# Kernel tuning notes

Measured on AMD Instinct MI355X. Metric: run time of the kernel, lower is better.

## Reference

```python
import jax, jax.numpy as jnp
import numpy as np

B, T, D, R, V = 8, 512, 1024, 4, 2048


def setup_inputs() -> dict:
    key = jax.random.key(0)
    k1, k2, k3, k4, k5 = jax.random.split(key, 5)
    return {
        "input_embs": jax.random.normal(k1, (B, T, D), dtype=jnp.float32),
        "label_ids": jax.random.randint(k2, (B, T), 0, V),
        "w_alpha": jax.random.normal(k3, (D, R), dtype=jnp.float32),
        "w_beta": jax.random.normal(k4, (D, R), dtype=jnp.float32),
        "w_vocab": jax.random.normal(k5, (D, V * R * R), dtype=jnp.float32),
    }


def _normalize(m, axis):
    # torch normalize_matrix: abs then divide by sum over `dim` (rows of the matrix)
    m = jnp.abs(m)
    return m / m.sum(axis=axis, keepdims=True)


def reference(input_embs, label_ids, w_alpha, w_beta, w_vocab):
    x = input_embs
    Bq, Tq, Dq = x.shape
    xf = x.reshape(-1, Dq)                                   # [B*T, D]
    alpha = (xf @ w_alpha).reshape(Bq, Tq, R).mean(1)        # [B, R]
    beta = (xf @ w_beta).reshape(Bq, Tq, R).mean(1)          # [B, R]
    core = (xf @ w_vocab).reshape(Bq, Tq, R, V, R).mean(1)   # [B, R, V, R]

    # gather core slices core[b, :, y[b,k], :] -> [B, T, R, R]
    g = jnp.take_along_axis(core.transpose(0, 2, 1, 3),      # [B, V, R, R]
                            label_ids[:, :, None, None], axis=1)
    Mn = _normalize(g, axis=2)                               # normalize over matrix rows (dim=0)

    v = _normalize(alpha, axis=1)                            # [B, R] normalized column vector
    Ms = Mn.transpose(1, 0, 2, 3)                            # [T, B, R, R]

    def step(v, M):
        return jnp.einsum('bij,bj->bi', M, v), None

    v, _ = jax.lax.scan(step, v, Ms)                         # sequential TT chain over T
    nb = _normalize(beta, axis=1)                            # [B, R]
    probs = jnp.einsum('bi,bi->b', nb, v)                    # [B]
    loss = -jnp.log(probs)
    return loss.mean()
```

## Files before the change

### kernel.cpp

```cpp
#include <hip/hip_runtime.h>
#include <math.h>

#define Bq 8
#define T 512
#define D 1024
#define R 4
#define V 2048
#define NCOL (V * R * R)
#define DSPLIT 16
#define DCHUNK (D / DSPLIT)
#define CBLK 1024

__global__ void k_xbar(const float* __restrict__ x, float* __restrict__ xbar) {
    int b   = blockIdx.x;
    int tc  = blockIdx.y;
    int tid = threadIdx.x;
    const float4* xp = (const float4*)(x + ((size_t)b * T + (size_t)tc * 16) * D) + tid;
    float4 acc = make_float4(0.f, 0.f, 0.f, 0.f);
#pragma unroll
    for (int t = 0; t < 16; ++t) {
        float4 v = xp[t * (D / 4)];
        acc.x += v.x; acc.y += v.y; acc.z += v.z; acc.w += v.w;
    }
    float* dst = xbar + b * D + tid * 4;
    atomicAdd(dst + 0, acc.x);
    atomicAdd(dst + 1, acc.y);
    atomicAdd(dst + 2, acc.z);
    atomicAdd(dst + 3, acc.w);
}

__global__ void k_core(const float* __restrict__ wv, const float* __restrict__ xbar,
                       float* __restrict__ part) {
    __shared__ float xs[Bq * DCHUNK];
    int tid  = threadIdx.x;
    int colb = blockIdx.x;
    int ds   = blockIdx.y;
    int d0   = ds * DCHUNK;

    if (tid < (Bq * DCHUNK / 4)) {
        int l  = tid * 4;
        int b  = l / DCHUNK;
        int dd = l % DCHUNK;
        *(float4*)(xs + l) = *(const float4*)(xbar + b * D + d0 + dd);
    }
    __syncthreads();

    int col = colb * CBLK + tid * 4;
    const float4* wp = (const float4*)(wv + (size_t)d0 * NCOL + col);
    float4 acc[Bq];
#pragma unroll
    for (int b = 0; b < Bq; ++b) acc[b] = make_float4(0.f, 0.f, 0.f, 0.f);

#pragma unroll 8
    for (int d = 0; d < DCHUNK; ++d) {
        float4 w = wp[(size_t)d * (NCOL / 4)];
#pragma unroll
        for (int b = 0; b < Bq; ++b) {
            float xv = xs[b * DCHUNK + d];
            acc[b].x += w.x * xv;
            acc[b].y += w.y * xv;
            acc[b].z += w.z * xv;
            acc[b].w += w.w * xv;
        }
    }

#pragma unroll
    for (int b = 0; b < Bq; ++b)
        *(float4*)(part + ((size_t)ds * Bq + b) * NCOL + col) = acc[b];
}

__global__ void k_gather(const float* __restrict__ part, const int* __restrict__ labels,
                         float* __restrict__ Mn) {
    int b   = blockIdx.x;
    int tc  = blockIdx.y;
    int tid = threadIdx.x;
    int tl  = tid >> 2;
    int i   = tid & 3;
    int t   = tc * 64 + tl;
    int y   = labels[b * T + t];

    const float* pb = part + (size_t)b * NCOL + (size_t)i * (V * R) + (size_t)y * R;
    float4 g = make_float4(0.f, 0.f, 0.f, 0.f);
#pragma unroll
    for (int ds = 0; ds < DSPLIT; ++ds) {
        float4 v = *(const float4*)(pb + (size_t)ds * (Bq * NCOL));
        g.x += v.x; g.y += v.y; g.z += v.z; g.w += v.w;
    }
    g.x = fabsf(g.x); g.y = fabsf(g.y); g.z = fabsf(g.z); g.w = fabsf(g.w);

    float sx = g.x, sy = g.y, sz = g.z, sw = g.w;
    sx += __shfl_xor(sx, 1); sy += __shfl_xor(sy, 1);
    sz += __shfl_xor(sz, 1); sw += __shfl_xor(sw, 1);
    sx += __shfl_xor(sx, 2); sy += __shfl_xor(sy, 2);
    sz += __shfl_xor(sz, 2); sw += __shfl_xor(sw, 2);

    float4 o = make_float4(g.x / sx, g.y / sy, g.z / sz, g.w / sw);
    *(float4*)(Mn + ((size_t)(b * T + t)) * 16 + i * 4) = o;
}

__global__ void k_chain(const float* __restrict__ Mn, const float* __restrict__ xbar,
                        const float* __restrict__ wa, const float* __restrict__ wb,
                        float* __restrict__ out) {
    __shared__ float mats[64][17];
    __shared__ float abp[64];
    int b   = blockIdx.x;
    int tid = threadIdx.x;

    {
        int r   = tid & 3;
        int sel = (tid >> 2) & 1;
        int seg = tid >> 3;
        const float* w  = sel ? wb : wa;
        const float* xp = xbar + b * D;
        float s = 0.f;
#pragma unroll 8
        for (int d = seg * 128; d < seg * 128 + 128; ++d)
            s += xp[d] * w[d * R + r];
        abp[tid] = s;
    }

    int c = tid;
    const float* mp = Mn + ((size_t)b * T + (size_t)c * 8) * 16;
    float P[R][R];
    {
        float4 m0 = *(const float4*)(mp + 0);
        float4 m1 = *(const float4*)(mp + 4);
        float4 m2 = *(const float4*)(mp + 8);
        float4 m3 = *(const float4*)(mp + 12);
        P[0][0]=m0.x; P[0][1]=m0.y; P[0][2]=m0.z; P[0][3]=m0.w;
        P[1][0]=m1.x; P[1][1]=m1.y; P[1][2]=m1.z; P[1][3]=m1.w;
        P[2][0]=m2.x; P[2][1]=m2.y; P[2][2]=m2.z; P[2][3]=m2.w;
        P[3][0]=m3.x; P[3][1]=m3.y; P[3][2]=m3.z; P[3][3]=m3.w;
    }
#pragma unroll
    for (int t = 1; t < 8; ++t) {
        float4 m0 = *(const float4*)(mp + t * 16 + 0);
        float4 m1 = *(const float4*)(mp + t * 16 + 4);
        float4 m2 = *(const float4*)(mp + t * 16 + 8);
        float4 m3 = *(const float4*)(mp + t * 16 + 12);
        float M[R][R] = {{m0.x, m0.y, m0.z, m0.w},
                         {m1.x, m1.y, m1.z, m1.w},
                         {m2.x, m2.y, m2.z, m2.w},
                         {m3.x, m3.y, m3.z, m3.w}};
        float N[R][R];
#pragma unroll
        for (int i = 0; i < R; ++i)
#pragma unroll
            for (int j = 0; j < R; ++j)
                N[i][j] = M[i][0] * P[0][j] + M[i][1] * P[1][j] +
                          M[i][2] * P[2][j] + M[i][3] * P[3][j];
#pragma unroll
        for (int i = 0; i < R; ++i)
#pragma unroll
            for (int j = 0; j < R; ++j) P[i][j] = N[i][j];
    }
#pragma unroll
    for (int i = 0; i < R; ++i)
#pragma unroll
        for (int j = 0; j < R; ++j) mats[c][i * 4 + j] = P[i][j];
    __syncthreads();

    for (int rnd = 0; rnd < 6; ++rnd) {
        int step = 1 << rnd;
        bool act = ((c & (2 * step - 1)) == 0);
        float N2[R][R];
        if (act) {
            float A[R][R], Bm[R][R];
#pragma unroll
            for (int i = 0; i < R; ++i)
#pragma unroll
                for (int j = 0; j < R; ++j) {
                    A[i][j]  = mats[c + step][i * 4 + j];
                    Bm[i][j] = mats[c][i * 4 + j];
                }
#pragma unroll
            for (int i = 0; i < R; ++i)
#pragma unroll
                for (int j = 0; j < R; ++j)
                    N2[i][j] = A[i][0] * Bm[0][j] + A[i][1] * Bm[1][j] +
                               A[i][2] * Bm[2][j] + A[i][3] * Bm[3][j];
        }
        __syncthreads();
        if (act) {
#pragma unroll
            for (int i = 0; i < R; ++i)
#pragma unroll
                for (int j = 0; j < R; ++j) mats[c][i * 4 + j] = N2[i][j];
        }
        __syncthreads();
    }

    if (tid == 0) {
        float a[R], be[R];
#pragma unroll
        for (int r = 0; r < R; ++r) {
            float sa = 0.f, sb = 0.f;
#pragma unroll
            for (int seg = 0; seg < 8; ++seg) {
                sa += abp[(seg << 3) | r];
                sb += abp[(seg << 3) | 4 | r];
            }
            a[r] = sa; be[r] = sb;
        }
        float sa = fabsf(a[0]) + fabsf(a[1]) + fabsf(a[2]) + fabsf(a[3]);
        float v0[R];
#pragma unroll
        for (int r = 0; r < R; ++r) v0[r] = fabsf(a[r]) / sa;
        float v[R];
#pragma unroll
        for (int i = 0; i < R; ++i)
            v[i] = mats[0][i * 4 + 0] * v0[0] + mats[0][i * 4 + 1] * v0[1] +
                   mats[0][i * 4 + 2] * v0[2] + mats[0][i * 4 + 3] * v0[3];
        float sb = fabsf(be[0]) + fabsf(be[1]) + fabsf(be[2]) + fabsf(be[3]);
        float prob = (fabsf(be[0]) * v[0] + fabsf(be[1]) * v[1] +
                      fabsf(be[2]) * v[2] + fabsf(be[3]) * v[3]) / sb;
        atomicAdd(out, -logf(prob) * 0.125f);
    }
}

extern "C" void kernel_launch(void* const* d_in, const int* in_sizes, int n_in,
                              void* d_out, int out_size, void* d_ws, size_t ws_size,
                              hipStream_t stream) {
    const float* x      = (const float*)d_in[0];
    const int*   labels = (const int*)d_in[1];
    const float* wa     = (const float*)d_in[2];
    const float* wb     = (const float*)d_in[3];
    const float* wv     = (const float*)d_in[4];
    float* out = (float*)d_out;

    float* xbar = (float*)d_ws;
    float* part = xbar + Bq * D;
    float* Mn   = part + (size_t)DSPLIT * Bq * NCOL;

    hipMemsetAsync(xbar, 0, Bq * D * sizeof(float), stream);
    hipMemsetAsync(out, 0, sizeof(float), stream);
    k_xbar<<<dim3(Bq, 32), 256, 0, stream>>>(x, xbar);
    k_core<<<dim3(NCOL / CBLK, DSPLIT), 256, 0, stream>>>(wv, xbar, part);
    k_gather<<<dim3(Bq, T / 64), 256, 0, stream>>>(part, labels, Mn);
    k_chain<<<Bq, 64, 0, stream>>>(Mn, xbar, wa, wb, out);
}
```

Baseline: 239.8 us.

## Fuse gather and chain kernels, halve D-split, drop output memset

Merges the gather/normalize kernel into the chain kernel: each batch block gathers its 512 normalized 4x4 matrices into shared memory and then runs the chain reduction, which removes the Mn global round trip and one launch. The D split is halved to 8 and the column block to 512 with 128-thread blocks, so the partial buffer written by the core GEMV and re-read by the gather is half the size. Zeroing the output moves into the first kernel, which removes one memset. The trade-off is that the fused kernel runs only 8 blocks, so the gather now has far less parallelism, and the core GEMV does longer per-thread reductions.

```diff
diff --git a/kernel.cpp b/kernel.cpp
--- a/kernel.cpp
+++ b/kernel.cpp
@@ -7,14 +7,16 @@
 #define R 4
 #define V 2048
 #define NCOL (V * R * R)
-#define DSPLIT 16
+#define DSPLIT 8
 #define DCHUNK (D / DSPLIT)
-#define CBLK 1024
-
-__global__ void k_xbar(const float* __restrict__ x, float* __restrict__ xbar) {
+#define CBLK 512
+
+__global__ void k_xbar(const float* __restrict__ x, float* __restrict__ xbar,
+                       float* __restrict__ out) {
     int b   = blockIdx.x;
     int tc  = blockIdx.y;
     int tid = threadIdx.x;
+    if (b == 0 && tc == 0 && tid == 0) out[0] = 0.f;
     const float4* xp = (const float4*)(x + ((size_t)b * T + (size_t)tc * 16) * D) + tid;
     float4 acc = make_float4(0.f, 0.f, 0.f, 0.f);
 #pragma unroll
@@ -37,11 +39,12 @@
     int ds   = blockIdx.y;
     int d0   = ds * DCHUNK;
 
-    if (tid < (Bq * DCHUNK / 4)) {
-        int l  = tid * 4;
-        int b  = l / DCHUNK;
-        int dd = l % DCHUNK;
-        *(float4*)(xs + l) = *(const float4*)(xbar + b * D + d0 + dd);
+    {
+        int l = tid * 8;
+        int b = tid >> 4;
+        int dd = l & (DCHUNK - 1);
+        *(float4*)(xs + l)     = *(const float4*)(xbar + b * D + d0 + dd);
+        *(float4*)(xs + l + 4) = *(const float4*)(xbar + b * D + d0 + dd + 4);
     }
     __syncthreads();
 
@@ -69,40 +72,13 @@
         *(float4*)(part + ((size_t)ds * Bq + b) * NCOL + col) = acc[b];
 }
 
-__global__ void k_gather(const float* __restrict__ part, const int* __restrict__ labels,
-                         float* __restrict__ Mn) {
-    int b   = blockIdx.x;
-    int tc  = blockIdx.y;
-    int tid = threadIdx.x;
-    int tl  = tid >> 2;
-    int i   = tid & 3;
-    int t   = tc * 64 + tl;
-    int y   = labels[b * T + t];
-
-    const float* pb = part + (size_t)b * NCOL + (size_t)i * (V * R) + (size_t)y * R;
-    float4 g = make_float4(0.f, 0.f, 0.f, 0.f);
-#pragma unroll
-    for (int ds = 0; ds < DSPLIT; ++ds) {
-        float4 v = *(const float4*)(pb + (size_t)ds * (Bq * NCOL));
-        g.x += v.x; g.y += v.y; g.z += v.z; g.w += v.w;
-    }
-    g.x = fabsf(g.x); g.y = fabsf(g.y); g.z = fabsf(g.z); g.w = fabsf(g.w);
-
-    float sx = g.x, sy = g.y, sz = g.z, sw = g.w;
-    sx += __shfl_xor(sx, 1); sy += __shfl_xor(sy, 1);
-    sz += __shfl_xor(sz, 1); sw += __shfl_xor(sw, 1);
-    sx += __shfl_xor(sx, 2); sy += __shfl_xor(sy, 2);
-    sz += __shfl_xor(sz, 2); sw += __shfl_xor(sw, 2);
-
-    float4 o = make_float4(g.x / sx, g.y / sy, g.z / sz, g.w / sw);
-    *(float4*)(Mn + ((size_t)(b * T + t)) * 16 + i * 4) = o;
-}
-
-__global__ void k_chain(const float* __restrict__ Mn, const float* __restrict__ xbar,
-                        const float* __restrict__ wa, const float* __restrict__ wb,
-                        float* __restrict__ out) {
+__global__ void k_fuse(const float* __restrict__ part, const int* __restrict__ labels,
+                       const float* __restrict__ xbar,
+                       const float* __restrict__ wa, const float* __restrict__ wb,
+                       float* __restrict__ out) {
+    __shared__ float Mn_s[T * 16];
     __shared__ float mats[64][17];
-    __shared__ float abp[64];
+    __shared__ float abp[256];
     int b   = blockIdx.x;
     int tid = threadIdx.x;
 
@@ -114,78 +90,106 @@
         const float* xp = xbar + b * D;
         float s = 0.f;
 #pragma unroll 8
-        for (int d = seg * 128; d < seg * 128 + 128; ++d)
+        for (int d = seg * 32; d < seg * 32 + 32; ++d)
             s += xp[d] * w[d * R + r];
         abp[tid] = s;
     }
 
+    int tl = tid >> 2;
+    int i  = tid & 3;
+#pragma unroll
+    for (int tc = 0; tc < 8; ++tc) {
+        int t = tc * 64 + tl;
+        int y = labels[b * T + t];
+        const float* pb = part + (size_t)b * NCOL + (size_t)i * (V * R) + (size_t)y * R;
+        float4 g = make_float4(0.f, 0.f, 0.f, 0.f);
+#pragma unroll
+        for (int ds = 0; ds < DSPLIT; ++ds) {
+            float4 v = *(const float4*)(pb + (size_t)ds * (Bq * NCOL));
+            g.x += v.x; g.y += v.y; g.z += v.z; g.w += v.w;
+        }
+        g.x = fabsf(g.x); g.y = fabsf(g.y); g.z = fabsf(g.z); g.w = fabsf(g.w);
+
+        float sx = g.x, sy = g.y, sz = g.z, sw = g.w;
+        sx += __shfl_xor(sx, 1); sy += __shfl_xor(sy, 1);
+        sz += __shfl_xor(sz, 1); sw += __shfl_xor(sw, 1);
+        sx += __shfl_xor(sx, 2); sy += __shfl_xor(sy, 2);
+        sz += __shfl_xor(sz, 2); sw += __shfl_xor(sw, 2);
+
+        float4 o = make_float4(g.x / sx, g.y / sy, g.z / sz, g.w / sw);
+        *(float4*)(Mn_s + t * 16 + i * 4) = o;
+    }
+    __syncthreads();
+
     int c = tid;
-    const float* mp = Mn + ((size_t)b * T + (size_t)c * 8) * 16;
     float P[R][R];
-    {
-        float4 m0 = *(const float4*)(mp + 0);
-        float4 m1 = *(const float4*)(mp + 4);
-        float4 m2 = *(const float4*)(mp + 8);
-        float4 m3 = *(const float4*)(mp + 12);
-        P[0][0]=m0.x; P[0][1]=m0.y; P[0][2]=m0.z; P[0][3]=m0.w;
-        P[1][0]=m1.x; P[1][1]=m1.y; P[1][2]=m1.z; P[1][3]=m1.w;
-        P[2][0]=m2.x; P[2][1]=m2.y; P[2][2]=m2.z; P[2][3]=m2.w;
-        P[3][0]=m3.x; P[3][1]=m3.y; P[3][2]=m3.z; P[3][3]=m3.w;
-    }
-#pragma unroll
-    for (int t = 1; t < 8; ++t) {
-        float4 m0 = *(const float4*)(mp + t * 16 + 0);
-        float4 m1 = *(const float4*)(mp + t * 16 + 4);
-        float4 m2 = *(const float4*)(mp + t * 16 + 8);
-        float4 m3 = *(const float4*)(mp + t * 16 + 12);
-        float M[R][R] = {{m0.x, m0.y, m0.z, m0.w},
-                         {m1.x, m1.y, m1.z, m1.w},
-                         {m2.x, m2.y, m2.z, m2.w},
-                         {m3.x, m3.y, m3.z, m3.w}};
-        float N[R][R];
-#pragma unroll
-        for (int i = 0; i < R; ++i)
-#pragma unroll
-            for (int j = 0; j < R; ++j)
-                N[i][j] = M[i][0] * P[0][j] + M[i][1] * P[1][j] +
-                          M[i][2] * P[2][j] + M[i][3] * P[3][j];
-#pragma unroll
-        for (int i = 0; i < R; ++i)
-#pragma unroll
-            for (int j = 0; j < R; ++j) P[i][j] = N[i][j];
-    }
-#pragma unroll
-    for (int i = 0; i < R; ++i)
-#pragma unroll
-        for (int j = 0; j < R; ++j) mats[c][i * 4 + j] = P[i][j];
+    if (c < 64) {
+        const float* mp = Mn_s + c * 8 * 16;
+        {
+            float4 m0 = *(const float4*)(mp + 0);
+            float4 m1 = *(const float4*)(mp + 4);
+            float4 m2 = *(const float4*)(mp + 8);
+            float4 m3 = *(const float4*)(mp + 12);
+            P[0][0]=m0.x; P[0][1]=m0.y; P[0][2]=m0.z; P[0][3]=m0.w;
+            P[1][0]=m1.x; P[1][1]=m1.y; P[1][2]=m1.z; P[1][3]=m1.w;
+            P[2][0]=m2.x; P[2][1]=m2.y; P[2][2]=m2.z; P[2][3]=m2.w;
+            P[3][0]=m3.x; P[3][1]=m3.y; P[3][2]=m3.z; P[3][3]=m3.w;
+        }
+#pragma unroll
+        for (int t = 1; t < 8; ++t) {
+            float4 m0 = *(const float4*)(mp + t * 16 + 0);
+            float4 m1 = *(const float4*)(mp + t * 16 + 4);
+            float4 m2 = *(const float4*)(mp + t * 16 + 8);
+            float4 m3 = *(const float4*)(mp + t * 16 + 12);
+            float M[R][R] = {{m0.x, m0.y, m0.z, m0.w},
+                             {m1.x, m1.y, m1.z, m1.w},
+                             {m2.x, m2.y, m2.z, m2.w},
+                             {m3.x, m3.y, m3.z, m3.w}};
+            float N[R][R];
+#pragma unroll
+            for (int ii = 0; ii < R; ++ii)
+#pragma unroll
+                for (int j = 0; j < R; ++j)
+                    N[ii][j] = M[ii][0] * P[0][j] + M[ii][1] * P[1][j] +
+                               M[ii][2] * P[2][j] + M[ii][3] * P[3][j];
+#pragma unroll
+            for (int ii = 0; ii < R; ++ii)
+#pragma unroll
+                for (int j = 0; j < R; ++j) P[ii][j] = N[ii][j];
+        }
+#pragma unroll
+        for (int ii = 0; ii < R; ++ii)
+#pragma unroll
+            for (int j = 0; j < R; ++j) mats[c][ii * 4 + j] = P[ii][j];
+    }
     __syncthreads();
 
     for (int rnd = 0; rnd < 6; ++rnd) {
         int step = 1 << rnd;
-        bool act = ((c & (2 * step - 1)) == 0);
+        bool act = (c < 64) && ((c & (2 * step - 1)) == 0);
         float N2[R][R];
         if (act) {
             float A[R][R], Bm[R][R];
 #pragma unroll
-            for (int i = 0; i < R; ++i)
+            for (int ii = 0; ii < R; ++ii)
 #pragma unroll
                 for (int j = 0; j < R; ++j) {
-                    A[i][j]  = mats[c + step][i * 4 + j];
-                    Bm[i][j] = mats[c][i * 4 + j];
+                    A[ii][j]  = mats[c + step][ii * 4 + j];
+                    Bm[ii][j] = mats[c][ii * 4 + j];
                 }
 #pragma unroll
-            for (int i = 0; i < R; ++i)
+            for (int ii = 0; ii < R; ++ii)
 #pragma unroll
                 for (int j = 0; j < R; ++j)
-                    N2[i][j] = A[i][0] * Bm[0][j] + A[i][1] * Bm[1][j] +
-                               A[i][2] * Bm[2][j] + A[i][3] * Bm[3][j];
+                    N2[ii][j] = A[ii][0] * Bm[0][j] + A[ii][1] * Bm[1][j] +
+                                A[ii][2] * Bm[2][j] + A[ii][3] * Bm[3][j];
         }
         __syncthreads();
         if (act) {
 #pragma unroll
-            for (int i = 0; i < R; ++i)
-#pragma unroll
-                for (int j = 0; j < R; ++j) mats[c][i * 4 + j] = N2[i][j];
+            for (int ii = 0; ii < R; ++ii)
+#pragma unroll
+                for (int j = 0; j < R; ++j) mats[c][ii * 4 + j] = N2[ii][j];
         }
         __syncthreads();
     }
@@ -195,8 +199,7 @@
 #pragma unroll
         for (int r = 0; r < R; ++r) {
             float sa = 0.f, sb = 0.f;
-#pragma unroll
-            for (int seg = 0; seg < 8; ++seg) {
+            for (int seg = 0; seg < 32; ++seg) {
                 sa += abp[(seg << 3) | r];
                 sb += abp[(seg << 3) | 4 | r];
             }
@@ -208,9 +211,9 @@
         for (int r = 0; r < R; ++r) v0[r] = fabsf(a[r]) / sa;
         float v[R];
 #pragma unroll
-        for (int i = 0; i < R; ++i)
-            v[i] = mats[0][i * 4 + 0] * v0[0] + mats[0][i * 4 + 1] * v0[1] +
-                   mats[0][i * 4 + 2] * v0[2] + mats[0][i * 4 + 3] * v0[3];
+        for (int ii = 0; ii < R; ++ii)
+            v[ii] = mats[0][ii * 4 + 0] * v0[0] + mats[0][ii * 4 + 1] * v0[1] +
+                    mats[0][ii * 4 + 2] * v0[2] + mats[0][ii * 4 + 3] * v0[3];
         float sb = fabsf(be[0]) + fabsf(be[1]) + fabsf(be[2]) + fabsf(be[3]);
         float prob = (fabsf(be[0]) * v[0] + fabsf(be[1]) * v[1] +
                       fabsf(be[2]) * v[2] + fabsf(be[3]) * v[3]) / sb;
@@ -230,12 +233,9 @@
 
     float* xbar = (float*)d_ws;
     float* part = xbar + Bq * D;
-    float* Mn   = part + (size_t)DSPLIT * Bq * NCOL;
 
     hipMemsetAsync(xbar, 0, Bq * D * sizeof(float), stream);
-    hipMemsetAsync(out, 0, sizeof(float), stream);
-    k_xbar<<<dim3(Bq, 32), 256, 0, stream>>>(x, xbar);
-    k_core<<<dim3(NCOL / CBLK, DSPLIT), 256, 0, stream>>>(wv, xbar, part);
-    k_gather<<<dim3(Bq, T / 64), 256, 0, stream>>>(part, labels, Mn);
-    k_chain<<<Bq, 64, 0, stream>>>(Mn, xbar, wa, wb, out);
-}
+    k_xbar<<<dim3(Bq, 32), 256, 0, stream>>>(x, xbar, out);
+    k_core<<<dim3(NCOL / CBLK, DSPLIT), 128, 0, stream>>>(wv, xbar, part);
+    k_fuse<<<Bq, 256, 0, stream>>>(part, labels, xbar, wa, wb, out);
+}
```

Result: slower. 247.9 us (+3.4%).

## Fuse four kernels into one cooperative kernel with grid-wide syncs

Applied to the files above, without the earlier changes.

Merges the xbar reduction, core GEMV, gather/normalize and chain kernels into a single cooperative launch of 512 blocks separated by grid.sync barriers. The output memset moves into the kernel. This removes three kernel launches and one memset. In exchange it adds grid-barrier cost and requires all 512 blocks to be co-resident. The out[0]=0 write by block 0 is ordered before the final atomicAdds only through the grid syncs.

```diff
diff --git a/kernel.cpp b/kernel.cpp
--- a/kernel.cpp
+++ b/kernel.cpp
@@ -1,5 +1,8 @@
 #include <hip/hip_runtime.h>
+#include <hip/hip_cooperative_groups.h>
 #include <math.h>
+
+namespace cg = cooperative_groups;
 
 #define Bq 8
 #define T 512
@@ -10,211 +13,220 @@
 #define DSPLIT 16
 #define DCHUNK (D / DSPLIT)
 #define CBLK 1024
-
-__global__ void k_xbar(const float* __restrict__ x, float* __restrict__ xbar) {
-    int b   = blockIdx.x;
-    int tc  = blockIdx.y;
-    int tid = threadIdx.x;
-    const float4* xp = (const float4*)(x + ((size_t)b * T + (size_t)tc * 16) * D) + tid;
-    float4 acc = make_float4(0.f, 0.f, 0.f, 0.f);
-#pragma unroll
-    for (int t = 0; t < 16; ++t) {
-        float4 v = xp[t * (D / 4)];
-        acc.x += v.x; acc.y += v.y; acc.z += v.z; acc.w += v.w;
-    }
-    float* dst = xbar + b * D + tid * 4;
-    atomicAdd(dst + 0, acc.x);
-    atomicAdd(dst + 1, acc.y);
-    atomicAdd(dst + 2, acc.z);
-    atomicAdd(dst + 3, acc.w);
-}
-
-__global__ void k_core(const float* __restrict__ wv, const float* __restrict__ xbar,
-                       float* __restrict__ part) {
+#define NBLK 512
+
+__global__ __launch_bounds__(256, 2) void k_mega(
+    const float* __restrict__ x, const int* __restrict__ labels,
+    const float* __restrict__ wa, const float* __restrict__ wb,
+    const float* __restrict__ wv, float* __restrict__ out,
+    float* __restrict__ xbar, float* __restrict__ part, float* __restrict__ Mn) {
+
+    cg::grid_group grid = cg::this_grid();
     __shared__ float xs[Bq * DCHUNK];
-    int tid  = threadIdx.x;
-    int colb = blockIdx.x;
-    int ds   = blockIdx.y;
-    int d0   = ds * DCHUNK;
-
-    if (tid < (Bq * DCHUNK / 4)) {
-        int l  = tid * 4;
-        int b  = l / DCHUNK;
-        int dd = l % DCHUNK;
-        *(float4*)(xs + l) = *(const float4*)(xbar + b * D + d0 + dd);
-    }
-    __syncthreads();
-
-    int col = colb * CBLK + tid * 4;
-    const float4* wp = (const float4*)(wv + (size_t)d0 * NCOL + col);
-    float4 acc[Bq];
-#pragma unroll
-    for (int b = 0; b < Bq; ++b) acc[b] = make_float4(0.f, 0.f, 0.f, 0.f);
-
-#pragma unroll 8
-    for (int d = 0; d < DCHUNK; ++d) {
-        float4 w = wp[(size_t)d * (NCOL / 4)];
-#pragma unroll
-        for (int b = 0; b < Bq; ++b) {
-            float xv = xs[b * DCHUNK + d];
-            acc[b].x += w.x * xv;
-            acc[b].y += w.y * xv;
-            acc[b].z += w.z * xv;
-            acc[b].w += w.w * xv;
-        }
-    }
-
-#pragma unroll
-    for (int b = 0; b < Bq; ++b)
-        *(float4*)(part + ((size_t)ds * Bq + b) * NCOL + col) = acc[b];
-}
-
-__global__ void k_gather(const float* __restrict__ part, const int* __restrict__ labels,
-                         float* __restrict__ Mn) {
-    int b   = blockIdx.x;
-    int tc  = blockIdx.y;
-    int tid = threadIdx.x;
-    int tl  = tid >> 2;
-    int i   = tid & 3;
-    int t   = tc * 64 + tl;
-    int y   = labels[b * T + t];
-
-    const float* pb = part + (size_t)b * NCOL + (size_t)i * (V * R) + (size_t)y * R;
-    float4 g = make_float4(0.f, 0.f, 0.f, 0.f);
-#pragma unroll
-    for (int ds = 0; ds < DSPLIT; ++ds) {
-        float4 v = *(const float4*)(pb + (size_t)ds * (Bq * NCOL));
-        g.x += v.x; g.y += v.y; g.z += v.z; g.w += v.w;
-    }
-    g.x = fabsf(g.x); g.y = fabsf(g.y); g.z = fabsf(g.z); g.w = fabsf(g.w);
-
-    float sx = g.x, sy = g.y, sz = g.z, sw = g.w;
-    sx += __shfl_xor(sx, 1); sy += __shfl_xor(sy, 1);
-    sz += __shfl_xor(sz, 1); sw += __shfl_xor(sw, 1);
-    sx += __shfl_xor(sx, 2); sy += __shfl_xor(sy, 2);
-    sz += __shfl_xor(sz, 2); sw += __shfl_xor(sw, 2);
-
-    float4 o = make_float4(g.x / sx, g.y / sy, g.z / sz, g.w / sw);
-    *(float4*)(Mn + ((size_t)(b * T + t)) * 16 + i * 4) = o;
-}
-
-__global__ void k_chain(const float* __restrict__ Mn, const float* __restrict__ xbar,
-                        const float* __restrict__ wa, const float* __restrict__ wb,
-                        float* __restrict__ out) {
     __shared__ float mats[64][17];
     __shared__ float abp[64];
-    int b   = blockIdx.x;
+    int blk = blockIdx.x;
     int tid = threadIdx.x;
 
+    if (blk == 0 && tid == 0) out[0] = 0.f;
+    if (blk < 256) {
+        int b  = blk >> 5;
+        int tc = blk & 31;
+        const float4* xp = (const float4*)(x + ((size_t)b * T + (size_t)tc * 16) * D) + tid;
+        float4 acc = make_float4(0.f, 0.f, 0.f, 0.f);
+#pragma unroll
+        for (int t = 0; t < 16; ++t) {
+            float4 v = xp[t * (D / 4)];
+            acc.x += v.x; acc.y += v.y; acc.z += v.z; acc.w += v.w;
+        }
+        float* dst = xbar + b * D + tid * 4;
+        atomicAdd(dst + 0, acc.x);
+        atomicAdd(dst + 1, acc.y);
+        atomicAdd(dst + 2, acc.z);
+        atomicAdd(dst + 3, acc.w);
+    }
+    grid.sync();
+
     {
-        int r   = tid & 3;
-        int sel = (tid >> 2) & 1;
-        int seg = tid >> 3;
-        const float* w  = sel ? wb : wa;
-        const float* xp = xbar + b * D;
-        float s = 0.f;
+        int colb = blk >> 4;
+        int ds   = blk & 15;
+        int d0   = ds * DCHUNK;
+
+        if (tid < 128) {
+            int q4 = tid * 4;
+            int b  = q4 >> 6;
+            int dd = q4 & 63;
+            *(float4*)(xs + q4) = *(const float4*)(xbar + b * D + d0 + dd);
+        }
+        __syncthreads();
+
+        int col = colb * CBLK + tid * 4;
+        const float4* wp = (const float4*)(wv + (size_t)d0 * NCOL + col);
+        float4 acc[Bq];
+#pragma unroll
+        for (int b = 0; b < Bq; ++b) acc[b] = make_float4(0.f, 0.f, 0.f, 0.f);
+
 #pragma unroll 8
-        for (int d = seg * 128; d < seg * 128 + 128; ++d)
-            s += xp[d] * w[d * R + r];
-        abp[tid] = s;
-    }
-
-    int c = tid;
-    const float* mp = Mn + ((size_t)b * T + (size_t)c * 8) * 16;
-    float P[R][R];
-    {
-        float4 m0 = *(const float4*)(mp + 0);
-        float4 m1 = *(const float4*)(mp + 4);
-        float4 m2 = *(const float4*)(mp + 8);
-        float4 m3 = *(const float4*)(mp + 12);
-        P[0][0]=m0.x; P[0][1]=m0.y; P[0][2]=m0.z; P[0][3]=m0.w;
-        P[1][0]=m1.x; P[1][1]=m1.y; P[1][2]=m1.z; P[1][3]=m1.w;
-        P[2][0]=m2.x; P[2][1]=m2.y; P[2][2]=m2.z; P[2][3]=m2.w;
-        P[3][0]=m3.x; P[3][1]=m3.y; P[3][2]=m3.z; P[3][3]=m3.w;
-    }
-#pragma unroll
-    for (int t = 1; t < 8; ++t) {
-        float4 m0 = *(const float4*)(mp + t * 16 + 0);
-        float4 m1 = *(const float4*)(mp + t * 16 + 4);
-        float4 m2 = *(const float4*)(mp + t * 16 + 8);
-        float4 m3 = *(const float4*)(mp + t * 16 + 12);
-        float M[R][R] = {{m0.x, m0.y, m0.z, m0.w},
-                         {m1.x, m1.y, m1.z, m1.w},
-                         {m2.x, m2.y, m2.z, m2.w},
-                         {m3.x, m3.y, m3.z, m3.w}};
-        float N[R][R];
-#pragma unroll
-        for (int i = 0; i < R; ++i)
-#pragma unroll
-            for (int j = 0; j < R; ++j)
-                N[i][j] = M[i][0] * P[0][j] + M[i][1] * P[1][j] +
-                          M[i][2] * P[2][j] + M[i][3] * P[3][j];
-#pragma unroll
-        for (int i = 0; i < R; ++i)
-#pragma unroll
-            for (int j = 0; j < R; ++j) P[i][j] = N[i][j];
-    }
-#pragma unroll
-    for (int i = 0; i < R; ++i)
-#pragma unroll
-        for (int j = 0; j < R; ++j) mats[c][i * 4 + j] = P[i][j];
-    __syncthreads();
-
-    for (int rnd = 0; rnd < 6; ++rnd) {
-        int step = 1 << rnd;
-        bool act = ((c & (2 * step - 1)) == 0);
-        float N2[R][R];
-        if (act) {
-            float A[R][R], Bm[R][R];
+        for (int d = 0; d < DCHUNK; ++d) {
+            float4 w = wp[(size_t)d * (NCOL / 4)];
+#pragma unroll
+            for (int b = 0; b < Bq; ++b) {
+                float xv = xs[b * DCHUNK + d];
+                acc[b].x += w.x * xv;
+                acc[b].y += w.y * xv;
+                acc[b].z += w.z * xv;
+                acc[b].w += w.w * xv;
+            }
+        }
+
+#pragma unroll
+        for (int b = 0; b < Bq; ++b)
+            *(float4*)(part + ((size_t)ds * Bq + b) * NCOL + col) = acc[b];
+    }
+    grid.sync();
+
+    if (blk < 64) {
+        int b  = blk >> 3;
+        int tc = blk & 7;
+        int tl = tid >> 2;
+        int i  = tid & 3;
+        int t  = tc * 64 + tl;
+        int y  = labels[b * T + t];
+
+        const float* pb = part + (size_t)b * NCOL + (size_t)i * (V * R) + (size_t)y * R;
+        float4 g = make_float4(0.f, 0.f, 0.f, 0.f);
+#pragma unroll
+        for (int ds = 0; ds < DSPLIT; ++ds) {
+            float4 v = *(const float4*)(pb + (size_t)ds * (Bq * NCOL));
+            g.x += v.x; g.y += v.y; g.z += v.z; g.w += v.w;
+        }
+        g.x = fabsf(g.x); g.y = fabsf(g.y); g.z = fabsf(g.z); g.w = fabsf(g.w);
+
+        float sx = g.x, sy = g.y, sz = g.z, sw = g.w;
+        sx += __shfl_xor(sx, 1); sy += __shfl_xor(sy, 1);
+        sz += __shfl_xor(sz, 1); sw += __shfl_xor(sw, 1);
+        sx += __shfl_xor(sx, 2); sy += __shfl_xor(sy, 2);
+        sz += __shfl_xor(sz, 2); sw += __shfl_xor(sw, 2);
+
+        float4 o = make_float4(g.x / sx, g.y / sy, g.z / sz, g.w / sw);
+        *(float4*)(Mn + ((size_t)(b * T + t)) * 16 + i * 4) = o;
+    }
+    grid.sync();
+
+    if (blk < Bq) {
+        int b = blk;
+        if (tid < 64) {
+            int r   = tid & 3;
+            int sel = (tid >> 2) & 1;
+            int seg = tid >> 3;
+            const float* w  = sel ? wb : wa;
+            const float* xp = xbar + b * D;
+            float s = 0.f;
+#pragma unroll 8
+            for (int d = seg * 128; d < seg * 128 + 128; ++d)
+                s += xp[d] * w[d * R + r];
+            abp[tid] = s;
+        }
+
+        int c = tid;
+        if (c < 64) {
+            const float* mp = Mn + ((size_t)b * T + (size_t)c * 8) * 16;
+            float P[R][R];
+            {
+                float4 m0 = *(const float4*)(mp + 0);
+                float4 m1 = *(const float4*)(mp + 4);
+                float4 m2 = *(const float4*)(mp + 8);
+                float4 m3 = *(const float4*)(mp + 12);
+                P[0][0]=m0.x; P[0][1]=m0.y; P[0][2]=m0.z; P[0][3]=m0.w;
+                P[1][0]=m1.x; P[1][1]=m1.y; P[1][2]=m1.z; P[1][3]=m1.w;
+                P[2][0]=m2.x; P[2][1]=m2.y; P[2][2]=m2.z; P[2][3]=m2.w;
+                P[3][0]=m3.x; P[3][1]=m3.y; P[3][2]=m3.z; P[3][3]=m3.w;
+            }
+#pragma unroll
+            for (int t = 1; t < 8; ++t) {
+                float4 m0 = *(const float4*)(mp + t * 16 + 0);
+                float4 m1 = *(const float4*)(mp + t * 16 + 4);
+                float4 m2 = *(const float4*)(mp + t * 16 + 8);
+                float4 m3 = *(const float4*)(mp + t * 16 + 12);
+                float M[R][R] = {{m0.x, m0.y, m0.z, m0.w},
+                                 {m1.x, m1.y, m1.z, m1.w},
+                                 {m2.x, m2.y, m2.z, m2.w},
+                                 {m3.x, m3.y, m3.z, m3.w}};
+                float N[R][R];
+#pragma unroll
+                for (int i = 0; i < R; ++i)
+#pragma unroll
+                    for (int j = 0; j < R; ++j)
+                        N[i][j] = M[i][0] * P[0][j] + M[i][1] * P[1][j] +
+                                  M[i][2] * P[2][j] + M[i][3] * P[3][j];
+#pragma unroll
+                for (int i = 0; i < R; ++i)
+#pragma unroll
+                    for (int j = 0; j < R; ++j) P[i][j] = N[i][j];
+            }
 #pragma unroll
             for (int i = 0; i < R; ++i)
 #pragma unroll
-                for (int j = 0; j < R; ++j) {
-                    A[i][j]  = mats[c + step][i * 4 + j];
-                    Bm[i][j] = mats[c][i * 4 + j];
+                for (int j = 0; j < R; ++j) mats[c][i * 4 + j] = P[i][j];
+        }
+        __syncthreads();
+
+        for (int rnd = 0; rnd < 6; ++rnd) {
+            int step = 1 << rnd;
+            bool act = (c < 64) && ((c & (2 * step - 1)) == 0);
+            float N2[R][R];
+            if (act) {
+                float A[R][R], Bm[R][R];
+#pragma unroll
+                for (int i = 0; i < R; ++i)
+#pragma unroll
+                    for (int j = 0; j < R; ++j) {
+                        A[i][j]  = mats[c + step][i * 4 + j];
+                        Bm[i][j] = mats[c][i * 4 + j];
+                    }
+#pragma unroll
+                for (int i = 0; i < R; ++i)
+#pragma unroll
+                    for (int j = 0; j < R; ++j)
+                        N2[i][j] = A[i][0] * Bm[0][j] + A[i][1] * Bm[1][j] +
+                                   A[i][2] * Bm[2][j] + A[i][3] * Bm[3][j];
+            }
+            __syncthreads();
+            if (act) {
+#pragma unroll
+                for (int i = 0; i < R; ++i)
+#pragma unroll
+                    for (int j = 0; j < R; ++j) mats[c][i * 4 + j] = N2[i][j];
+            }
+            __syncthreads();
+        }
+
+        if (tid == 0) {
+            float a[R], be[R];
+#pragma unroll
+            for (int r = 0; r < R; ++r) {
+                float sa = 0.f, sb = 0.f;
+#pragma unroll
+                for (int seg = 0; seg < 8; ++seg) {
+                    sa += abp[(seg << 3) | r];
+                    sb += abp[(seg << 3) | 4 | r];
                 }
+                a[r] = sa; be[r] = sb;
+            }
+            float sa = fabsf(a[0]) + fabsf(a[1]) + fabsf(a[2]) + fabsf(a[3]);
+            float v0[R];
+#pragma unroll
+            for (int r = 0; r < R; ++r) v0[r] = fabsf(a[r]) / sa;
+            float v[R];
 #pragma unroll
             for (int i = 0; i < R; ++i)
-#pragma unroll
-                for (int j = 0; j < R; ++j)
-                    N2[i][j] = A[i][0] * Bm[0][j] + A[i][1] * Bm[1][j] +
-                               A[i][2] * Bm[2][j] + A[i][3] * Bm[3][j];
-        }
-        __syncthreads();
-        if (act) {
-#pragma unroll
-            for (int i = 0; i < R; ++i)
-#pragma unroll
-                for (int j = 0; j < R; ++j) mats[c][i * 4 + j] = N2[i][j];
-        }
-        __syncthreads();
-    }
-
-    if (tid == 0) {
-        float a[R], be[R];
-#pragma unroll
-        for (int r = 0; r < R; ++r) {
-            float sa = 0.f, sb = 0.f;
-#pragma unroll
-            for (int seg = 0; seg < 8; ++seg) {
-                sa += abp[(seg << 3) | r];
-                sb += abp[(seg << 3) | 4 | r];
-            }
-            a[r] = sa; be[r] = sb;
-        }
-        float sa = fabsf(a[0]) + fabsf(a[1]) + fabsf(a[2]) + fabsf(a[3]);
-        float v0[R];
-#pragma unroll
-        for (int r = 0; r < R; ++r) v0[r] = fabsf(a[r]) / sa;
-        float v[R];
-#pragma unroll
-        for (int i = 0; i < R; ++i)
-            v[i] = mats[0][i * 4 + 0] * v0[0] + mats[0][i * 4 + 1] * v0[1] +
-                   mats[0][i * 4 + 2] * v0[2] + mats[0][i * 4 + 3] * v0[3];
-        float sb = fabsf(be[0]) + fabsf(be[1]) + fabsf(be[2]) + fabsf(be[3]);
-        float prob = (fabsf(be[0]) * v[0] + fabsf(be[1]) * v[1] +
-                      fabsf(be[2]) * v[2] + fabsf(be[3]) * v[3]) / sb;
-        atomicAdd(out, -logf(prob) * 0.125f);
+                v[i] = mats[0][i * 4 + 0] * v0[0] + mats[0][i * 4 + 1] * v0[1] +
+                       mats[0][i * 4 + 2] * v0[2] + mats[0][i * 4 + 3] * v0[3];
+            float sb = fabsf(be[0]) + fabsf(be[1]) + fabsf(be[2]) + fabsf(be[3]);
+            float prob = (fabsf(be[0]) * v[0] + fabsf(be[1]) * v[1] +
+                          fabsf(be[2]) * v[2] + fabsf(be[3]) * v[3]) / sb;
+            atomicAdd(out, -logf(prob) * 0.125f);
+        }
     }
 }
 
@@ -233,9 +245,9 @@
     float* Mn   = part + (size_t)DSPLIT * Bq * NCOL;
 
     hipMemsetAsync(xbar, 0, Bq * D * sizeof(float), stream);
-    hipMemsetAsync(out, 0, sizeof(float), stream);
-    k_xbar<<<dim3(Bq, 32), 256, 0, stream>>>(x, xbar);
-    k_core<<<dim3(NCOL / CBLK, DSPLIT), 256, 0, stream>>>(wv, xbar, part);
-    k_gather<<<dim3(Bq, T / 64), 256, 0, stream>>>(part, labels, Mn);
-    k_chain<<<Bq, 64, 0, stream>>>(Mn, xbar, wa, wb, out);
+
+    void* args[] = {(void*)&x, (void*)&labels, (void*)&wa, (void*)&wb,
+                    (void*)&wv, (void*)&out, (void*)&xbar, (void*)&part, (void*)&Mn};
+    hipLaunchCooperativeKernel((const void*)k_mega, dim3(NBLK), dim3(256),
+                               args, 0, stream);
 }
```

Result: slower. 415.1 us (+73.1%).
